# Optimization experiments

Hardware: AMD Instinct MI355X
Metric: run time of the kernel (lower is better)

Reference implementation:

```python
import jax, jax.numpy as jnp
import numpy as np

N, E, D = 50000, 600000, 128
NUM_BOND_TYPE, NUM_BOND_DIR = 5, 3
SELF_LOOP_TYPE = 4  # self-loop edge_attr = [4, 0]


def setup_inputs() -> dict:
    key = jax.random.key(0)
    ks = jax.random.split(key, 10)
    x = jax.random.normal(ks[0], (N, D), dtype=jnp.float32)
    edge_index = jax.random.randint(ks[1], (2, E), 0, N, dtype=jnp.int64)
    edge_attr = jax.random.randint(ks[2], (E, 2), 0, 3, dtype=jnp.int64)
    # learned params (torch Linear: y = x @ W.T + b)
    s1 = 1.0 / np.sqrt(D)
    s2 = 1.0 / np.sqrt(2 * D)
    W1 = jax.random.uniform(ks[3], (2 * D, D), jnp.float32, -s1, s1)
    b1 = jax.random.uniform(ks[4], (2 * D,), jnp.float32, -s1, s1)
    W2 = jax.random.uniform(ks[5], (D, 2 * D), jnp.float32, -s2, s2)
    b2 = jax.random.uniform(ks[6], (D,), jnp.float32, -s2, s2)
    e1 = jax.random.normal(ks[7], (NUM_BOND_TYPE, D), jnp.float32) * np.sqrt(2.0 / (NUM_BOND_TYPE + D))
    e2 = jax.random.normal(ks[8], (NUM_BOND_DIR, D), jnp.float32) * np.sqrt(2.0 / (NUM_BOND_DIR + D))
    return {"x": x, "edge_index": edge_index, "edge_attr": edge_attr,
            "W1": W1, "b1": b1, "W2": W2, "b2": b2, "e1": e1, "e2": e2}


def reference(x, edge_index, edge_attr, W1, b1, W2, b2, e1, e2):
    row, col = edge_index[0], edge_index[1]
    # edge embeddings for the real edges: [E, D]
    edge_emb = e1[edge_attr[:, 0]] + e2[edge_attr[:, 1]]
    # messages gathered from source nodes, scatter-added to destinations
    messages = x[col] + edge_emb  # [E, D]
    out = jax.ops.segment_sum(messages, row, num_segments=N)
    # self-loops: add_self_loops appends edge (i,i) with attr [4,0] for each node,
    # contributing x[i] + e1[4] + e2[0] to out[i]; add it directly (same math).
    out = out + x + e1[SELF_LOOP_TYPE] + e2[0]
    # 2-layer MLP
    h = jax.nn.relu(out @ W1.T + b1)
    return h @ W2.T + b2
```

## Files before the change

### kernel.cpp

```cpp
#include <hip/hip_runtime.h>

#define N_NODES 50000
#define N_EDGES 600000
#define DIM 128

#define CAP 64
#define GRID_E 2344
#define BLK_ROWS 16
#define GRID_FUSED 3125

#define DUMMY (50000u | (5u << 16) | (3u << 19))

#define WS_CNT_OFF   0
#define WS_PERM_OFF  200000
#define WS_XB_OFF    13000000
#define WS_W1B_OFF   25800256
#define WS_W2B_OFF   25865792

#define CVT_X4    1600000
#define CVT_XROWS 1600032
#define CVT_W4    8192
#define CVT_TOTAL (CVT_XROWS + 2 * CVT_W4)
#define CVT_BLOCKS ((CVT_TOTAL + 255) / 256)
#define ZERO_BLOCKS 196

typedef __attribute__((ext_vector_type(8))) short bf16x8;
typedef __attribute__((ext_vector_type(4))) float f32x4;

__device__ __forceinline__ unsigned short f2bf(float f) {
    unsigned int b = __float_as_uint(f);
    b += 0x7FFFu + ((b >> 16) & 1u);
    return (unsigned short)(b >> 16);
}
__device__ __forceinline__ float bf2f(short u) {
    return __uint_as_float(((unsigned int)(unsigned short)u) << 16);
}

__global__ __launch_bounds__(256) void place_kernel(
    const int* __restrict__ eidx, const int* __restrict__ eattr,
    int* __restrict__ cnt, unsigned int* __restrict__ perm)
{
    int e = blockIdx.x * 256 + threadIdx.x;
    if (e >= N_EDGES) return;
    int row = eidx[e];
    unsigned int col = (unsigned int)eidx[N_EDGES + e];
    unsigned int a0  = (unsigned int)eattr[2 * e];
    unsigned int a1  = (unsigned int)eattr[2 * e + 1];
    int pos = atomicAdd(&cnt[row], 1);
    if (pos < CAP)
        perm[(size_t)row * CAP + pos] = col | (a0 << 16) | (a1 << 19);
}

__global__ __launch_bounds__(256) void cvt_all_kernel(
    const float* __restrict__ x, const float* __restrict__ W1,
    const float* __restrict__ W2, unsigned short* __restrict__ xb,
    unsigned short* __restrict__ w1b, unsigned short* __restrict__ w2b,
    int* __restrict__ cnt)
{
    if (blockIdx.x >= CVT_BLOCKS) {
        int j = (blockIdx.x - CVT_BLOCKS) * 256 + threadIdx.x;
        if (j < N_NODES) cnt[j] = 0;
        return;
    }
    int i = blockIdx.x * 256 + threadIdx.x;
    if (i < CVT_X4) {
        float4 v = reinterpret_cast<const float4*>(x)[i];
        reinterpret_cast<ushort4*>(xb)[i] =
            make_ushort4(f2bf(v.x), f2bf(v.y), f2bf(v.z), f2bf(v.w));
    } else if (i < CVT_XROWS) {
        reinterpret_cast<ushort4*>(xb)[i] = make_ushort4(0, 0, 0, 0);
    } else if (i < CVT_XROWS + CVT_W4) {
        int j = i - CVT_XROWS;
        float4 v = reinterpret_cast<const float4*>(W1)[j];
        reinterpret_cast<ushort4*>(w1b)[j] =
            make_ushort4(f2bf(v.x), f2bf(v.y), f2bf(v.z), f2bf(v.w));
    } else if (i < CVT_TOTAL) {
        int j = i - CVT_XROWS - CVT_W4;
        float4 v = reinterpret_cast<const float4*>(W2)[j];
        reinterpret_cast<ushort4*>(w2b)[j] =
            make_ushort4(f2bf(v.x), f2bf(v.y), f2bf(v.z), f2bf(v.w));
    }
}

__global__ __launch_bounds__(256) void fused_mlp_kernel(
    const float* __restrict__ x, const unsigned short* __restrict__ xb,
    const float* __restrict__ e1, const float* __restrict__ e2,
    const unsigned int* __restrict__ perm, const int* __restrict__ cnt,
    const unsigned short* __restrict__ w1b, const float* __restrict__ b1,
    const unsigned short* __restrict__ w2b, const float* __restrict__ b2,
    float* __restrict__ Y)
{
    __shared__ __align__(16) unsigned short sA[16][136];
    __shared__ __align__(16) unsigned short sH[16][264];

    int t = threadIdx.x;

    {
        int n  = t >> 4;
        int g  = blockIdx.x * BLK_ROWS + n;
        int ln = t & 15, c0 = ln * 8;

        const float* xr = x + (size_t)g * DIM + c0;
        float4 s0 = *reinterpret_cast<const float4*>(xr);
        float4 s1 = *reinterpret_cast<const float4*>(xr + 4);

        int ne = cnt[g]; if (ne > CAP) ne = CAP;
        const uint4* pp4 = reinterpret_cast<const uint4*>(perm + (size_t)g * CAP);

        unsigned long long c0v = 1ull << 48;
        unsigned int       c1v = 1u;
        float acc[8] = {0.f, 0.f, 0.f, 0.f, 0.f, 0.f, 0.f, 0.f};

        for (int e = 0; e < ne; e += 8) {
            int i0 = e >> 2;
            uint4 a = pp4[i0];
            uint4 b = pp4[i0 + 1];
            unsigned ua[8] = {a.x, a.y, a.z, a.w, b.x, b.y, b.z, b.w};
            #pragma unroll
            for (int q = 0; q < 8; ++q)
                if (e + q >= ne) ua[q] = DUMMY;
            bf16x8 xv[8];
            #pragma unroll
            for (int q = 0; q < 8; ++q)
                xv[q] = *reinterpret_cast<const bf16x8*>(
                    xb + (size_t)(ua[q] & 0xFFFFu) * DIM + c0);
            #pragma unroll
            for (int q = 0; q < 8; ++q) {
                c0v += 1ull << (12 * ((ua[q] >> 16) & 7u));
                c1v += 1u   << (10 * (ua[q] >> 19));
            }
            #pragma unroll
            for (int j = 0; j < 8; ++j)
                acc[j] += ((bf2f(xv[0][j]) + bf2f(xv[1][j])) +
                           (bf2f(xv[2][j]) + bf2f(xv[3][j]))) +
                          ((bf2f(xv[4][j]) + bf2f(xv[5][j])) +
                           (bf2f(xv[6][j]) + bf2f(xv[7][j])));
        }

        acc[0] += s0.x; acc[1] += s0.y; acc[2] += s0.z; acc[3] += s0.w;
        acc[4] += s1.x; acc[5] += s1.y; acc[6] += s1.z; acc[7] += s1.w;

        #pragma unroll
        for (int tt = 0; tt < 5; ++tt) {
            float m = (float)((unsigned int)((c0v >> (12 * tt)) & 0xFFFu));
            const float* er = e1 + tt * DIM + c0;
            float4 u0 = *reinterpret_cast<const float4*>(er);
            float4 u1 = *reinterpret_cast<const float4*>(er + 4);
            acc[0] += m * u0.x; acc[1] += m * u0.y;
            acc[2] += m * u0.z; acc[3] += m * u0.w;
            acc[4] += m * u1.x; acc[5] += m * u1.y;
            acc[6] += m * u1.z; acc[7] += m * u1.w;
        }
        #pragma unroll
        for (int tt = 0; tt < 3; ++tt) {
            float m = (float)((c1v >> (10 * tt)) & 0x3FFu);
            const float* er = e2 + tt * DIM + c0;
            float4 u0 = *reinterpret_cast<const float4*>(er);
            float4 u1 = *reinterpret_cast<const float4*>(er + 4);
            acc[0] += m * u0.x; acc[1] += m * u0.y;
            acc[2] += m * u0.z; acc[3] += m * u0.w;
            acc[4] += m * u1.x; acc[5] += m * u1.y;
            acc[6] += m * u1.z; acc[7] += m * u1.w;
        }

        bf16x8 o;
        #pragma unroll
        for (int j = 0; j < 8; ++j) o[j] = (short)f2bf(acc[j]);
        *reinterpret_cast<bf16x8*>(&sA[n][c0]) = o;
    }
    __syncthreads();

    int wid = t >> 6;
    int l   = t & 63;
    int l16 = l & 15;
    int lhi = l >> 4;
    int rowbase = blockIdx.x * BLK_ROWS;

    bf16x8 af[4];
    #pragma unroll
    for (int kk = 0; kk < 4; ++kk)
        af[kk] = *reinterpret_cast<const bf16x8*>(&sA[l16][kk * 32 + lhi * 8]);

    float tb1[4];
    #pragma unroll
    for (int i = 0; i < 4; ++i) tb1[i] = b1[(wid * 4 + i) * 16 + l16];

    f32x4 acc1[4];
    #pragma unroll
    for (int i = 0; i < 4; ++i) acc1[i] = (f32x4){0.f, 0.f, 0.f, 0.f};

    #pragma unroll
    for (int kk = 0; kk < 4; ++kk) {
        bf16x8 wf[4];
        #pragma unroll
        for (int i = 0; i < 4; ++i)
            wf[i] = *reinterpret_cast<const bf16x8*>(
                w1b + (size_t)((wid * 4 + i) * 16 + l16) * DIM + kk * 32 + lhi * 8);
        #pragma unroll
        for (int i = 0; i < 4; ++i)
            acc1[i] = __builtin_amdgcn_mfma_f32_16x16x32_bf16(af[kk], wf[i], acc1[i], 0, 0, 0);
    }
    #pragma unroll
    for (int i = 0; i < 4; ++i) {
        int n0 = (wid * 4 + i) * 16;
        #pragma unroll
        for (int r = 0; r < 4; ++r)
            sH[lhi * 4 + r][n0 + l16] = f2bf(fmaxf(acc1[i][r] + tb1[i], 0.f));
    }
    __syncthreads();

    float tb2[2];
    #pragma unroll
    for (int i = 0; i < 2; ++i) tb2[i] = b2[(wid * 2 + i) * 16 + l16];

    f32x4 acc2[2];
    #pragma unroll
    for (int i = 0; i < 2; ++i) acc2[i] = (f32x4){0.f, 0.f, 0.f, 0.f};

    #pragma unroll
    for (int kk = 0; kk < 8; ++kk) {
        bf16x8 hf = *reinterpret_cast<const bf16x8*>(&sH[l16][kk * 32 + lhi * 8]);
        bf16x8 wf[2];
        #pragma unroll
        for (int i = 0; i < 2; ++i)
            wf[i] = *reinterpret_cast<const bf16x8*>(
                w2b + (size_t)((wid * 2 + i) * 16 + l16) * 256 + kk * 32 + lhi * 8);
        #pragma unroll
        for (int i = 0; i < 2; ++i)
            acc2[i] = __builtin_amdgcn_mfma_f32_16x16x32_bf16(hf, wf[i], acc2[i], 0, 0, 0);
    }
    #pragma unroll
    for (int i = 0; i < 2; ++i) {
        int n0 = (wid * 2 + i) * 16;
        #pragma unroll
        for (int r = 0; r < 4; ++r)
            Y[(size_t)(rowbase + lhi * 4 + r) * DIM + n0 + l16] = acc2[i][r] + tb2[i];
    }
}

extern "C" void kernel_launch(void* const* d_in, const int* in_sizes, int n_in,
                              void* d_out, int out_size, void* d_ws, size_t ws_size,
                              hipStream_t stream)
{
    const float* x   = (const float*)d_in[0];
    const int*  eidx = (const int*)d_in[1];
    const int*  eattr= (const int*)d_in[2];
    const float* W1  = (const float*)d_in[3];
    const float* b1  = (const float*)d_in[4];
    const float* W2  = (const float*)d_in[5];
    const float* b2  = (const float*)d_in[6];
    const float* e1  = (const float*)d_in[7];
    const float* e2  = (const float*)d_in[8];
    float* Y = (float*)d_out;

    char* ws = (char*)d_ws;
    int* cnt             = (int*)(ws + WS_CNT_OFF);
    unsigned int* perm   = (unsigned int*)(ws + WS_PERM_OFF);
    unsigned short* xb   = (unsigned short*)(ws + WS_XB_OFF);
    unsigned short* w1b  = (unsigned short*)(ws + WS_W1B_OFF);
    unsigned short* w2b  = (unsigned short*)(ws + WS_W2B_OFF);

    cvt_all_kernel  <<<CVT_BLOCKS + ZERO_BLOCKS, 256, 0, stream>>>(
                        x, W1, W2, xb, w1b, w2b, cnt);
    place_kernel    <<<GRID_E, 256, 0, stream>>>(eidx, eattr, cnt, perm);
    fused_mlp_kernel<<<GRID_FUSED, 256, 0, stream>>>(
                        x, xb, e1, e2, perm, cnt, w1b, b1, w2b, b2, Y);
}
```

Before: 118.7 us.

## Merge conversion and edge placement into one prep kernel, prefetch gather batches

The cnt zeroing moves to hipMemsetAsync, and the bf16 conversion and edge-bucketing work are merged into a single prep kernel, so two dependent launches become one and both jobs run concurrently. The gather loop in the fused MLP kernel is software-pipelined: it loads the next batch of 8 neighbour rows before reducing the current one, hiding memory latency. Launch bounds are raised to request 4 blocks per CU. The prefetch doubles the live bf16 vectors, which adds register pressure, and the memset adds an extra stream operation.

```diff
diff --git a/kernel.cpp b/kernel.cpp
--- a/kernel.cpp
+++ b/kernel.cpp
@@ -21,8 +21,8 @@
 #define CVT_XROWS 1600032
 #define CVT_W4    8192
 #define CVT_TOTAL (CVT_XROWS + 2 * CVT_W4)
-#define CVT_BLOCKS ((CVT_TOTAL + 255) / 256)
-#define ZERO_BLOCKS 196
+#define CVT_BLOCKS 6315
+#define PREP_GRID (CVT_BLOCKS + GRID_E)
 
 typedef __attribute__((ext_vector_type(8))) short bf16x8;
 typedef __attribute__((ext_vector_type(4))) float f32x4;
@@ -36,30 +36,23 @@
     return __uint_as_float(((unsigned int)(unsigned short)u) << 16);
 }
 
-__global__ __launch_bounds__(256) void place_kernel(
-    const int* __restrict__ eidx, const int* __restrict__ eattr,
+__global__ __launch_bounds__(256) void prep_kernel(
+    const float* __restrict__ x, const float* __restrict__ W1,
+    const float* __restrict__ W2, const int* __restrict__ eidx,
+    const int* __restrict__ eattr, unsigned short* __restrict__ xb,
+    unsigned short* __restrict__ w1b, unsigned short* __restrict__ w2b,
     int* __restrict__ cnt, unsigned int* __restrict__ perm)
 {
-    int e = blockIdx.x * 256 + threadIdx.x;
-    if (e >= N_EDGES) return;
-    int row = eidx[e];
-    unsigned int col = (unsigned int)eidx[N_EDGES + e];
-    unsigned int a0  = (unsigned int)eattr[2 * e];
-    unsigned int a1  = (unsigned int)eattr[2 * e + 1];
-    int pos = atomicAdd(&cnt[row], 1);
-    if (pos < CAP)
-        perm[(size_t)row * CAP + pos] = col | (a0 << 16) | (a1 << 19);
-}
-
-__global__ __launch_bounds__(256) void cvt_all_kernel(
-    const float* __restrict__ x, const float* __restrict__ W1,
-    const float* __restrict__ W2, unsigned short* __restrict__ xb,
-    unsigned short* __restrict__ w1b, unsigned short* __restrict__ w2b,
-    int* __restrict__ cnt)
-{
     if (blockIdx.x >= CVT_BLOCKS) {
-        int j = (blockIdx.x - CVT_BLOCKS) * 256 + threadIdx.x;
-        if (j < N_NODES) cnt[j] = 0;
+        int e = (blockIdx.x - CVT_BLOCKS) * 256 + threadIdx.x;
+        if (e >= N_EDGES) return;
+        int row = eidx[e];
+        unsigned int col = (unsigned int)eidx[N_EDGES + e];
+        unsigned int a0  = (unsigned int)eattr[2 * e];
+        unsigned int a1  = (unsigned int)eattr[2 * e + 1];
+        int pos = atomicAdd(&cnt[row], 1);
+        if (pos < CAP)
+            perm[(size_t)row * CAP + pos] = col | (a0 << 16) | (a1 << 19);
         return;
     }
     int i = blockIdx.x * 256 + threadIdx.x;
@@ -82,7 +75,7 @@
     }
 }
 
-__global__ __launch_bounds__(256) void fused_mlp_kernel(
+__global__ __launch_bounds__(256, 4) void fused_mlp_kernel(
     const float* __restrict__ x, const unsigned short* __restrict__ xb,
     const float* __restrict__ e1, const float* __restrict__ e2,
     const unsigned int* __restrict__ perm, const int* __restrict__ cnt,
@@ -111,30 +104,51 @@
         unsigned int       c1v = 1u;
         float acc[8] = {0.f, 0.f, 0.f, 0.f, 0.f, 0.f, 0.f, 0.f};
 
+        unsigned cur[8];
+        bf16x8 xcur[8];
+        {
+            uint4 pa = pp4[0], pb = pp4[1];
+            cur[0] = pa.x; cur[1] = pa.y; cur[2] = pa.z; cur[3] = pa.w;
+            cur[4] = pb.x; cur[5] = pb.y; cur[6] = pb.z; cur[7] = pb.w;
+            #pragma unroll
+            for (int q = 0; q < 8; ++q) if (q >= ne) cur[q] = DUMMY;
+            #pragma unroll
+            for (int q = 0; q < 8; ++q)
+                xcur[q] = *reinterpret_cast<const bf16x8*>(
+                    xb + (size_t)(cur[q] & 0xFFFFu) * DIM + c0);
+        }
+
         for (int e = 0; e < ne; e += 8) {
-            int i0 = e >> 2;
-            uint4 a = pp4[i0];
-            uint4 b = pp4[i0 + 1];
-            unsigned ua[8] = {a.x, a.y, a.z, a.w, b.x, b.y, b.z, b.w};
-            #pragma unroll
-            for (int q = 0; q < 8; ++q)
-                if (e + q >= ne) ua[q] = DUMMY;
-            bf16x8 xv[8];
-            #pragma unroll
-            for (int q = 0; q < 8; ++q)
-                xv[q] = *reinterpret_cast<const bf16x8*>(
-                    xb + (size_t)(ua[q] & 0xFFFFu) * DIM + c0);
+            const bool more = (e + 8) < ne;
+            unsigned nxt[8];
+            bf16x8 xnxt[8];
+            if (more) {
+                int i0 = (e >> 2) + 2;
+                uint4 pa = pp4[i0], pb = pp4[i0 + 1];
+                nxt[0] = pa.x; nxt[1] = pa.y; nxt[2] = pa.z; nxt[3] = pa.w;
+                nxt[4] = pb.x; nxt[5] = pb.y; nxt[6] = pb.z; nxt[7] = pb.w;
+                #pragma unroll
+                for (int q = 0; q < 8; ++q) if (e + 8 + q >= ne) nxt[q] = DUMMY;
+                #pragma unroll
+                for (int q = 0; q < 8; ++q)
+                    xnxt[q] = *reinterpret_cast<const bf16x8*>(
+                        xb + (size_t)(nxt[q] & 0xFFFFu) * DIM + c0);
+            }
             #pragma unroll
             for (int q = 0; q < 8; ++q) {
-                c0v += 1ull << (12 * ((ua[q] >> 16) & 7u));
-                c1v += 1u   << (10 * (ua[q] >> 19));
+                c0v += 1ull << (12 * ((cur[q] >> 16) & 7u));
+                c1v += 1u   << (10 * (cur[q] >> 19));
             }
             #pragma unroll
             for (int j = 0; j < 8; ++j)
-                acc[j] += ((bf2f(xv[0][j]) + bf2f(xv[1][j])) +
-                           (bf2f(xv[2][j]) + bf2f(xv[3][j]))) +
-                          ((bf2f(xv[4][j]) + bf2f(xv[5][j])) +
-                           (bf2f(xv[6][j]) + bf2f(xv[7][j])));
+                acc[j] += ((bf2f(xcur[0][j]) + bf2f(xcur[1][j])) +
+                           (bf2f(xcur[2][j]) + bf2f(xcur[3][j]))) +
+                          ((bf2f(xcur[4][j]) + bf2f(xcur[5][j])) +
+                           (bf2f(xcur[6][j]) + bf2f(xcur[7][j])));
+            if (more) {
+                #pragma unroll
+                for (int q = 0; q < 8; ++q) { cur[q] = nxt[q]; xcur[q] = xnxt[q]; }
+            }
         }
 
         acc[0] += s0.x; acc[1] += s0.y; acc[2] += s0.z; acc[3] += s0.w;
@@ -260,9 +274,9 @@
     unsigned short* w1b  = (unsigned short*)(ws + WS_W1B_OFF);
     unsigned short* w2b  = (unsigned short*)(ws + WS_W2B_OFF);
 
-    cvt_all_kernel  <<<CVT_BLOCKS + ZERO_BLOCKS, 256, 0, stream>>>(
-                        x, W1, W2, xb, w1b, w2b, cnt);
-    place_kernel    <<<GRID_E, 256, 0, stream>>>(eidx, eattr, cnt, perm);
+    hipMemsetAsync(cnt, 0, N_NODES * sizeof(int), stream);
+    prep_kernel     <<<PREP_GRID, 256, 0, stream>>>(
+                        x, W1, W2, eidx, eattr, xb, w1b, w2b, cnt, perm);
     fused_mlp_kernel<<<GRID_FUSED, 256, 0, stream>>>(
                         x, xb, e1, e2, perm, cnt, w1b, b1, w2b, b2, Y);
 }
```

Measured after the change: 134.2 us. 1.13x slower.
